# Performance work log

Hardware: AMD Instinct MI355X
Metric: run time of the kernel (lower is better)

Reference implementation:

```python
import jax, jax.numpy as jnp
import numpy as np

B, N, C = 16, 1024, 1152
H = 16
D = C // H  # 72
INNER = 4608
EPS = 1e-6


def _layernorm(x, g, b):
    mu = jnp.mean(x, axis=-1, keepdims=True)
    var = jnp.mean(jnp.square(x - mu), axis=-1, keepdims=True)
    return (x - mu) * jax.lax.rsqrt(var + EPS) * g + b


def setup_inputs() -> dict:
    key = jax.random.key(0)
    ks = jax.random.split(key, 16)
    s_c = 1.0 / np.sqrt(C)
    s_i = 1.0 / np.sqrt(INNER)
    return {
        "x": jax.random.normal(ks[0], (B, N, C), dtype=jnp.float32),
        "ln1_g": jnp.ones((C,), jnp.float32),
        "ln1_b": jnp.zeros((C,), jnp.float32),
        # weights stored (in, out) so y = x @ W + b (equiv to torch x @ W.T + b)
        "qkv_w": jax.random.normal(ks[1], (C, 3 * C), jnp.float32) * s_c,
        "qkv_b": jnp.zeros((3 * C,), jnp.float32),
        "proj_w": jax.random.normal(ks[2], (C, C), jnp.float32) * s_c,
        "proj_b": jnp.zeros((C,), jnp.float32),
        "ln2_g": jnp.ones((C,), jnp.float32),
        "ln2_b": jnp.zeros((C,), jnp.float32),
        "fc1_w": jax.random.normal(ks[3], (C, INNER), jnp.float32) * s_c,
        "fc1_b": jnp.zeros((INNER,), jnp.float32),
        "fc2_w": jax.random.normal(ks[4], (INNER, C), jnp.float32) * s_i,
        "fc2_b": jnp.zeros((C,), jnp.float32),
    }


def reference(x, ln1_g, ln1_b, qkv_w, qkv_b, proj_w, proj_b,
              ln2_g, ln2_b, fc1_w, fc1_b, fc2_w, fc2_b):
    scale = D ** -0.5
    # --- attention branch ---
    h = _layernorm(x, ln1_g, ln1_b)
    qkv = (h @ qkv_w + qkv_b).reshape(B, N, 3, H, D)
    q, k, v = jnp.moveaxis(qkv, 2, 0)            # each (B, N, H, D)
    q = q.transpose(0, 2, 1, 3)                   # (B, H, N, D)
    k = k.transpose(0, 2, 1, 3)
    v = v.transpose(0, 2, 1, 3)
    attn = jnp.einsum('bhnd,bhmd->bhnm', q, k) * scale
    attn = jax.nn.softmax(attn, axis=-1)
    out = jnp.einsum('bhnm,bhmd->bhnd', attn, v)
    out = out.transpose(0, 2, 1, 3).reshape(B, N, C)
    x = x + out @ proj_w + proj_b
    # --- MLP branch ---
    h = _layernorm(x, ln2_g, ln2_b)
    h = jax.nn.gelu(h @ fc1_w + fc1_b, approximate=False)
    x = x + h @ fc2_w + fc2_b
    return x
```

## Files before the change

### kernel.cpp

```cpp
#include <hip/hip_runtime.h>
#include <hip/hip_bf16.h>

typedef unsigned short ushort_t;
using short8 = __attribute__((ext_vector_type(8))) short;
using f32x4  = __attribute__((ext_vector_type(4))) float;

#define DEVI __device__ __forceinline__

DEVI ushort_t f2bf(float f) {
    union { float f; unsigned u; } c; c.f = f;
    unsigned u = c.u;
    return (ushort_t)((u + 0x7FFF + ((u >> 16) & 1)) >> 16);
}

DEVI f32x4 mfma16(short8 a, short8 b, f32x4 c) {
    return __builtin_amdgcn_mfma_f32_16x16x32_bf16(a, b, c, 0, 0, 0);
}

DEVI void gld16(const void* g, void* l) {
    __builtin_amdgcn_global_load_lds(
        (const __attribute__((address_space(1))) unsigned int*)g,
        (__attribute__((address_space(3))) unsigned int*)l, 16, 0, 0);
}

#define Bsz 16
#define Ntok 1024
#define Cdim 1152
#define Hn 16
#define Dh 72
#define Dp 96
#define INNER 4608
#define Mrows (Bsz * Ntok)

#define OFF_QKV_WT  ((size_t)0)
#define OFF_PROJ_WT ((size_t)7962624)
#define OFF_FC1_WT  ((size_t)10616832)
#define OFF_FC2_WT  ((size_t)21233664)
#define OFF_H       ((size_t)31850496)
#define OFF_ATT     ((size_t)69599232)
#define OFF_Q       ((size_t)107347968)
#define OFF_K       ((size_t)157679616)
#define OFF_VT      ((size_t)208011264)
#define OFF_HIDDEN  OFF_Q

__global__ __launch_bounds__(256) void transpose_cast(
    const float* __restrict__ W, ushort_t* __restrict__ Wt, int K, int N)
{
    __shared__ float t[64][65];
    const int n0 = blockIdx.x * 64;
    const int k0 = blockIdx.y * 64;
    #pragma unroll
    for (int j = 0; j < 4; ++j) {
        int idx = threadIdx.x + j * 256;
        int r = idx >> 4;
        int c4 = idx & 15;
        float4 v = *(const float4*)&W[(size_t)(k0 + r) * N + n0 + c4 * 4];
        t[r][c4 * 4 + 0] = v.x; t[r][c4 * 4 + 1] = v.y;
        t[r][c4 * 4 + 2] = v.z; t[r][c4 * 4 + 3] = v.w;
    }
    __syncthreads();
    #pragma unroll
    for (int j = 0; j < 4; ++j) {
        int idx = threadIdx.x + j * 256;
        int rn = idx >> 4;
        int c4 = idx & 15;
        ushort4 o;
        o.x = f2bf(t[c4 * 4 + 0][rn]);
        o.y = f2bf(t[c4 * 4 + 1][rn]);
        o.z = f2bf(t[c4 * 4 + 2][rn]);
        o.w = f2bf(t[c4 * 4 + 3][rn]);
        *(ushort4*)&Wt[(size_t)(n0 + rn) * K + k0 + c4 * 4] = o;
    }
}

__global__ __launch_bounds__(256) void ln_kernel(
    const float* __restrict__ x, const float* __restrict__ g,
    const float* __restrict__ b, ushort_t* __restrict__ out)
{
    const int row = blockIdx.x;
    const int tid = threadIdx.x;
    const int lane = tid & 63, wid = tid >> 6;
    const float* xr = x + (size_t)row * Cdim;

    float4 v0 = ((const float4*)xr)[tid];
    float4 v1 = {0, 0, 0, 0};
    if (tid < 32) v1 = ((const float4*)xr)[256 + tid];
    float s  = v0.x + v0.y + v0.z + v0.w + v1.x + v1.y + v1.z + v1.w;
    float s2 = v0.x*v0.x + v0.y*v0.y + v0.z*v0.z + v0.w*v0.w
             + v1.x*v1.x + v1.y*v1.y + v1.z*v1.z + v1.w*v1.w;
    #pragma unroll
    for (int off = 32; off >= 1; off >>= 1) {
        s  += __shfl_xor(s, off);
        s2 += __shfl_xor(s2, off);
    }
    __shared__ float red[8];
    if (lane == 0) { red[wid] = s; red[4 + wid] = s2; }
    __syncthreads();
    s  = red[0] + red[1] + red[2] + red[3];
    s2 = red[4] + red[5] + red[6] + red[7];
    const float mu = s * (1.0f / Cdim);
    const float var = s2 * (1.0f / Cdim) - mu * mu;
    const float rs = rsqrtf(var + 1e-6f);

    ushort_t* orow = out + (size_t)row * Cdim;
    {
        float4 g4 = ((const float4*)g)[tid];
        float4 b4 = ((const float4*)b)[tid];
        ushort4 o;
        o.x = f2bf((v0.x - mu) * rs * g4.x + b4.x);
        o.y = f2bf((v0.y - mu) * rs * g4.y + b4.y);
        o.z = f2bf((v0.z - mu) * rs * g4.z + b4.z);
        o.w = f2bf((v0.w - mu) * rs * g4.w + b4.w);
        ((ushort4*)orow)[tid] = o;
    }
    if (tid < 32) {
        float4 g4 = ((const float4*)g)[256 + tid];
        float4 b4 = ((const float4*)b)[256 + tid];
        ushort4 o;
        o.x = f2bf((v1.x - mu) * rs * g4.x + b4.x);
        o.y = f2bf((v1.y - mu) * rs * g4.y + b4.y);
        o.z = f2bf((v1.z - mu) * rs * g4.z + b4.z);
        o.w = f2bf((v1.w - mu) * rs * g4.w + b4.w);
        ((ushort4*)orow)[256 + tid] = o;
    }
}

enum { EPI_QKV = 0, EPI_PROJ = 1, EPI_FC1 = 2, EPI_FC2 = 3 };

template<int EPI, int N, int K>
__global__ __launch_bounds__(256) void gemm_bt(
    const ushort_t* __restrict__ A, const ushort_t* __restrict__ Bt,
    const float* __restrict__ bias, const float* __restrict__ resid,
    float* __restrict__ outf, ushort_t* __restrict__ outb,
    ushort_t* __restrict__ outq, ushort_t* __restrict__ outk, ushort_t* __restrict__ outv)
{
    __shared__ ushort_t As[128 * 32];
    __shared__ ushort_t Bs[128 * 32];
    const int tid = threadIdx.x;
    const int lane = tid & 63, wid = tid >> 6;
    const int m0 = blockIdx.y * 128;
    const int n0 = blockIdx.x * 128;
    const int fr = lane & 15, fq = lane >> 4;

    f32x4 acc[4][4] = {};

    const int srow = lane >> 2;
    const int scol = (lane & 3) * 8;
    const ushort_t* Ag = A + (size_t)m0 * K;
    const ushort_t* Bg = Bt + (size_t)n0 * K;

    for (int kk = 0; kk < K; kk += 32) {
        #pragma unroll
        for (int j = 0; j < 2; ++j) {
            const int crow = wid * 32 + j * 16;
            gld16(Ag + (size_t)(crow + srow) * K + kk + scol, &As[crow * 32]);
            gld16(Bg + (size_t)(crow + srow) * K + kk + scol, &Bs[crow * 32]);
        }
        __syncthreads();
        short8 af[4], bfr[4];
        #pragma unroll
        for (int mi = 0; mi < 4; ++mi)
            af[mi] = *(const short8*)&As[((wid >> 1) * 64 + mi * 16 + fr) * 32 + fq * 8];
        #pragma unroll
        for (int ni = 0; ni < 4; ++ni)
            bfr[ni] = *(const short8*)&Bs[((wid & 1) * 64 + ni * 16 + fr) * 32 + fq * 8];
        #pragma unroll
        for (int mi = 0; mi < 4; ++mi)
            #pragma unroll
            for (int ni = 0; ni < 4; ++ni)
                acc[mi][ni] = mfma16(af[mi], bfr[ni], acc[mi][ni]);
        __syncthreads();
    }

    #pragma unroll
    for (int mi = 0; mi < 4; ++mi) {
        #pragma unroll
        for (int ni = 0; ni < 4; ++ni) {
            const int col = n0 + (wid & 1) * 64 + ni * 16 + fr;
            const int rbase = m0 + (wid >> 1) * 64 + mi * 16 + fq * 4;
            #pragma unroll
            for (int i = 0; i < 4; ++i) {
                const int r = rbase + i;
                float v = acc[mi][ni][i];
                if (EPI == EPI_QKV) {
                    v += bias[col];
                    const int which = col / Cdim;
                    const int rc = col % Cdim;
                    const int h = rc / Dh, d = rc % Dh;
                    const int b = r >> 10, n = r & 1023;
                    const size_t head = (size_t)(b * Hn + h);
                    if (which == 0)      outq[(head * Ntok + n) * Dp + d] = f2bf(v);
                    else if (which == 1) outk[(head * Ntok + n) * Dp + d] = f2bf(v);
                    else                 outv[(head * Dp + d) * Ntok + n] = f2bf(v);
                } else if (EPI == EPI_PROJ) {
                    v += bias[col] + resid[(size_t)r * N + col];
                    outf[(size_t)r * N + col] = v;
                } else if (EPI == EPI_FC1) {
                    v += bias[col];
                    v = 0.5f * v * (1.0f + erff(v * 0.70710678118f));
                    outb[(size_t)r * N + col] = f2bf(v);
                } else {
                    v += bias[col] + outf[(size_t)r * N + col];
                    outf[(size_t)r * N + col] = v;
                }
            }
        }
    }
}

__global__ __launch_bounds__(256) void attn_kernel(
    const ushort_t* __restrict__ q, const ushort_t* __restrict__ k,
    const ushort_t* __restrict__ vt, ushort_t* __restrict__ out)
{
    const int tid = threadIdx.x;
    const int lane = tid & 63, wid = tid >> 6;
    const int bh = blockIdx.y;
    const int qbase = blockIdx.x * 128 + wid * 32;
    const int fr = lane & 15, fq = lane >> 4;
    const ushort_t* qh = q  + (size_t)bh * Ntok * Dp;
    const ushort_t* kh = k  + (size_t)bh * Ntok * Dp;
    const ushort_t* vh = vt + (size_t)bh * Dp * Ntok;

    short8 aq[2][3];
    #pragma unroll
    for (int t = 0; t < 2; ++t)
        #pragma unroll
        for (int ks = 0; ks < 3; ++ks)
            aq[t][ks] = *(const short8*)&qh[(size_t)(qbase + t * 16 + fr) * Dp + ks * 32 + fq * 8];

    f32x4 o[2][5] = {};
    float mrun[2][4], lsum[2][4];
    #pragma unroll
    for (int t = 0; t < 2; ++t)
        #pragma unroll
        for (int i = 0; i < 4; ++i) { mrun[t][i] = -1e30f; lsum[t][i] = 0.0f; }

    __shared__ ushort_t plds[4][2][16][32];
    const float scale = 0.117851130f;

    for (int kv = 0; kv < Ntok; kv += 32) {
        short8 kb0[3], kb1[3], bv[5];
        #pragma unroll
        for (int ks = 0; ks < 3; ++ks) {
            kb0[ks] = *(const short8*)&kh[(size_t)(kv + fr) * Dp + ks * 32 + fq * 8];
            kb1[ks] = *(const short8*)&kh[(size_t)(kv + 16 + fr) * Dp + ks * 32 + fq * 8];
        }
        #pragma unroll
        for (int dt = 0; dt < 5; ++dt)
            bv[dt] = *(const short8*)&vh[(size_t)(dt * 16 + fr) * Ntok + kv + fq * 8];

        f32x4 s[2][2] = {};
        __builtin_amdgcn_s_setprio(1);
        #pragma unroll
        for (int ks = 0; ks < 3; ++ks)
            #pragma unroll
            for (int t = 0; t < 2; ++t) {
                s[t][0] = mfma16(aq[t][ks], kb0[ks], s[t][0]);
                s[t][1] = mfma16(aq[t][ks], kb1[ks], s[t][1]);
            }
        __builtin_amdgcn_s_setprio(0);

        #pragma unroll
        for (int t = 0; t < 2; ++t) {
            float a0[4], a1[4];
            float lmax = -1e30f;
            #pragma unroll
            for (int i = 0; i < 4; ++i) {
                a0[i] = s[t][0][i] * scale;
                a1[i] = s[t][1][i] * scale;
                lmax = fmaxf(lmax, fmaxf(a0[i], a1[i]));
            }
            const float mmin = fminf(fminf(mrun[t][0], mrun[t][1]),
                                     fminf(mrun[t][2], mrun[t][3]));
            if (!__all(lmax <= mmin + 8.0f)) {
                #pragma unroll
                for (int i = 0; i < 4; ++i) {
                    float mx = fmaxf(a0[i], a1[i]);
                    mx = fmaxf(mx, __shfl_xor(mx, 1));
                    mx = fmaxf(mx, __shfl_xor(mx, 2));
                    mx = fmaxf(mx, __shfl_xor(mx, 4));
                    mx = fmaxf(mx, __shfl_xor(mx, 8));
                    const float mnew = fmaxf(mrun[t][i], mx);
                    const float f = __expf(mrun[t][i] - mnew);
                    mrun[t][i] = mnew;
                    lsum[t][i] *= f;
                    #pragma unroll
                    for (int dt = 0; dt < 5; ++dt) o[t][dt][i] *= f;
                }
            }
            #pragma unroll
            for (int i = 0; i < 4; ++i) {
                float p0 = __expf(a0[i] - mrun[t][i]);
                float p1 = __expf(a1[i] - mrun[t][i]);
                lsum[t][i] += p0 + p1;
                plds[wid][t][fq * 4 + i][fr]      = f2bf(p0);
                plds[wid][t][fq * 4 + i][16 + fr] = f2bf(p1);
            }
        }
        short8 pa[2];
        #pragma unroll
        for (int t = 0; t < 2; ++t)
            pa[t] = *(const short8*)&plds[wid][t][fr][fq * 8];
        __builtin_amdgcn_s_setprio(1);
        #pragma unroll
        for (int dt = 0; dt < 5; ++dt)
            #pragma unroll
            for (int t = 0; t < 2; ++t)
                o[t][dt] = mfma16(pa[t], bv[dt], o[t][dt]);
        __builtin_amdgcn_s_setprio(0);
    }

    const int b = bh >> 4, h = bh & 15;
    #pragma unroll
    for (int t = 0; t < 2; ++t) {
        float inv[4];
        #pragma unroll
        for (int i = 0; i < 4; ++i) {
            float s = lsum[t][i];
            s += __shfl_xor(s, 1);
            s += __shfl_xor(s, 2);
            s += __shfl_xor(s, 4);
            s += __shfl_xor(s, 8);
            inv[i] = 1.0f / s;
        }
        #pragma unroll
        for (int dt = 0; dt < 5; ++dt) {
            const int d = dt * 16 + fr;
            if (d < Dh) {
                #pragma unroll
                for (int i = 0; i < 4; ++i) {
                    const size_t idx = ((size_t)(b * Ntok) + qbase + t * 16 + fq * 4 + i) * Cdim + h * Dh + d;
                    out[idx] = f2bf(o[t][dt][i] * inv[i]);
                }
            }
        }
    }
}

extern "C" void kernel_launch(void* const* d_in, const int* in_sizes, int n_in,
                              void* d_out, int out_size, void* d_ws, size_t ws_size,
                              hipStream_t stream) {
    const float* x      = (const float*)d_in[0];
    const float* ln1_g  = (const float*)d_in[1];
    const float* ln1_b  = (const float*)d_in[2];
    const float* qkv_w  = (const float*)d_in[3];
    const float* qkv_b  = (const float*)d_in[4];
    const float* proj_w = (const float*)d_in[5];
    const float* proj_b = (const float*)d_in[6];
    const float* ln2_g  = (const float*)d_in[7];
    const float* ln2_b  = (const float*)d_in[8];
    const float* fc1_w  = (const float*)d_in[9];
    const float* fc1_b  = (const float*)d_in[10];
    const float* fc2_w  = (const float*)d_in[11];
    const float* fc2_b  = (const float*)d_in[12];

    char* ws = (char*)d_ws;
    ushort_t* qkv_wT  = (ushort_t*)(ws + OFF_QKV_WT);
    ushort_t* proj_wT = (ushort_t*)(ws + OFF_PROJ_WT);
    ushort_t* fc1_wT  = (ushort_t*)(ws + OFF_FC1_WT);
    ushort_t* fc2_wT  = (ushort_t*)(ws + OFF_FC2_WT);
    ushort_t* hbuf    = (ushort_t*)(ws + OFF_H);
    ushort_t* attnout = (ushort_t*)(ws + OFF_ATT);
    ushort_t* qb      = (ushort_t*)(ws + OFF_Q);
    ushort_t* kb      = (ushort_t*)(ws + OFF_K);
    ushort_t* vtb     = (ushort_t*)(ws + OFF_VT);
    ushort_t* hidden  = (ushort_t*)(ws + OFF_HIDDEN);
    float* out = (float*)d_out;

    hipMemsetAsync(ws + OFF_Q, 0, (size_t)3 * 50331648, stream);

    transpose_cast<<<dim3(3 * Cdim / 64, Cdim / 64), 256, 0, stream>>>(qkv_w, qkv_wT, Cdim, 3 * Cdim);
    transpose_cast<<<dim3(Cdim / 64, Cdim / 64), 256, 0, stream>>>(proj_w, proj_wT, Cdim, Cdim);
    transpose_cast<<<dim3(INNER / 64, Cdim / 64), 256, 0, stream>>>(fc1_w, fc1_wT, Cdim, INNER);
    transpose_cast<<<dim3(Cdim / 64, INNER / 64), 256, 0, stream>>>(fc2_w, fc2_wT, INNER, Cdim);

    ln_kernel<<<Mrows, 256, 0, stream>>>(x, ln1_g, ln1_b, hbuf);

    gemm_bt<EPI_QKV, 3 * Cdim, Cdim><<<dim3(27, 128), 256, 0, stream>>>(
        hbuf, qkv_wT, qkv_b, nullptr, nullptr, nullptr, qb, kb, vtb);

    attn_kernel<<<dim3(Ntok / 128, Bsz * Hn), 256, 0, stream>>>(qb, kb, vtb, attnout);

    gemm_bt<EPI_PROJ, Cdim, Cdim><<<dim3(9, 128), 256, 0, stream>>>(
        attnout, proj_wT, proj_b, x, out, nullptr, nullptr, nullptr, nullptr);

    ln_kernel<<<Mrows, 256, 0, stream>>>(out, ln2_g, ln2_b, hbuf);

    gemm_bt<EPI_FC1, INNER, Cdim><<<dim3(36, 128), 256, 0, stream>>>(
        hbuf, fc1_wT, fc1_b, nullptr, nullptr, hidden, nullptr, nullptr, nullptr);

    gemm_bt<EPI_FC2, Cdim, INNER><<<dim3(9, 128), 256, 0, stream>>>(
        hidden, fc2_wT, fc2_b, nullptr, out, nullptr, nullptr, nullptr, nullptr);
}
```

Baseline: 1.233 ms.

## Rework GEMM to 256x128x64 tiles with triple-buffered async LDS pipeline and swizzle

The bf16 GEMM kernel now uses 512-thread blocks with 256x128 output tiles and a K-step of 64. Global-to-LDS loads are triple-buffered so the loads for tile t+2 are in flight while tile t is computed, using explicit vmcnt waits. The LDS layout is XOR-swizzled to avoid bank conflicts, and MFMA issue runs at raised priority. The aim is to hide memory latency and cut barrier overhead and LDS traffic per FLOP, at the cost of 144KB of LDS per block, which limits occupancy, and more intricate synchronization.

```diff
diff --git a/kernel.cpp b/kernel.cpp
--- a/kernel.cpp
+++ b/kernel.cpp
@@ -127,57 +127,113 @@
 
 enum { EPI_QKV = 0, EPI_PROJ = 1, EPI_FC1 = 2, EPI_FC2 = 3 };
 
+#define TBM 256
+#define TBN 128
+#define TBK 64
+#define BUFB 49152
+
 template<int EPI, int N, int K>
-__global__ __launch_bounds__(256) void gemm_bt(
+__global__ __launch_bounds__(512, 2) void gemm_bt(
     const ushort_t* __restrict__ A, const ushort_t* __restrict__ Bt,
     const float* __restrict__ bias, const float* __restrict__ resid,
     float* __restrict__ outf, ushort_t* __restrict__ outb,
     ushort_t* __restrict__ outq, ushort_t* __restrict__ outk, ushort_t* __restrict__ outv)
 {
-    __shared__ ushort_t As[128 * 32];
-    __shared__ ushort_t Bs[128 * 32];
+    __shared__ ushort_t smem[3 * BUFB / 2];
     const int tid = threadIdx.x;
     const int lane = tid & 63, wid = tid >> 6;
-    const int m0 = blockIdx.y * 128;
-    const int n0 = blockIdx.x * 128;
+    const int wr = wid >> 1, wc = wid & 1;
     const int fr = lane & 15, fq = lane >> 4;
-
-    f32x4 acc[4][4] = {};
-
-    const int srow = lane >> 2;
-    const int scol = (lane & 3) * 8;
+    const int m0 = blockIdx.y * TBM;
+    const int n0 = blockIdx.x * TBN;
+
     const ushort_t* Ag = A + (size_t)m0 * K;
     const ushort_t* Bg = Bt + (size_t)n0 * K;
 
-    for (int kk = 0; kk < K; kk += 32) {
-        #pragma unroll
-        for (int j = 0; j < 2; ++j) {
-            const int crow = wid * 32 + j * 16;
-            gld16(Ag + (size_t)(crow + srow) * K + kk + scol, &As[crow * 32]);
-            gld16(Bg + (size_t)(crow + srow) * K + kk + scol, &Bs[crow * 32]);
-        }
-        __syncthreads();
-        short8 af[4], bfr[4];
-        #pragma unroll
-        for (int mi = 0; mi < 4; ++mi)
-            af[mi] = *(const short8*)&As[((wid >> 1) * 64 + mi * 16 + fr) * 32 + fq * 8];
-        #pragma unroll
-        for (int ni = 0; ni < 4; ++ni)
-            bfr[ni] = *(const short8*)&Bs[((wid & 1) * 64 + ni * 16 + fr) * 32 + fq * 8];
-        #pragma unroll
-        for (int mi = 0; mi < 4; ++mi)
-            #pragma unroll
-            for (int ni = 0; ni < 4; ++ni)
-                acc[mi][ni] = mfma16(af[mi], bfr[ni], acc[mi][ni]);
-        __syncthreads();
-    }
+    size_t srcA[4]; int dstA[4];
+    #pragma unroll
+    for (int r = 0; r < 4; ++r) {
+        const int chunk = r * 512 + tid;
+        const int row = chunk >> 3;
+        const int slot = chunk & 7;
+        srcA[r] = (size_t)row * K + (slot ^ (row & 7)) * 8;
+        dstA[r] = (r * 512 + wid * 64) * 16;
+    }
+    size_t srcB[2]; int dstB[2];
+    #pragma unroll
+    for (int r = 0; r < 2; ++r) {
+        const int chunk = r * 512 + tid;
+        const int row = chunk >> 3;
+        const int slot = chunk & 7;
+        srcB[r] = (size_t)row * K + (slot ^ (row & 7)) * 8;
+        dstB[r] = 32768 + (r * 512 + wid * 64) * 16;
+    }
+
+    auto STAGE = [&](int buf, int kk) {
+        char* lb = (char*)smem + (size_t)buf * BUFB;
+        #pragma unroll
+        for (int r = 0; r < 4; ++r) gld16(Ag + srcA[r] + kk, lb + dstA[r]);
+        #pragma unroll
+        for (int r = 0; r < 2; ++r) gld16(Bg + srcB[r] + kk, lb + dstB[r]);
+    };
+
+    const int swz = (fr & 7) << 4;
+    int aoff[4][2], boff[4][2];
+    #pragma unroll
+    for (int i = 0; i < 4; ++i)
+        #pragma unroll
+        for (int kh = 0; kh < 2; ++kh) {
+            const int rowA = wr * 64 + i * 16 + fr;
+            aoff[i][kh] = rowA * 128 + ((kh * 64 + fq * 16) ^ swz);
+            const int rowB = wc * 64 + i * 16 + fr;
+            boff[i][kh] = 32768 + rowB * 128 + ((kh * 64 + fq * 16) ^ swz);
+        }
+
+    f32x4 acc[4][4] = {};
+    const int NT = K / TBK;
+
+    STAGE(0, 0);
+    STAGE(1, TBK);
+
+    auto COMPUTE = [&](int t) {
+        const char* lb = (const char*)smem + (size_t)(t % 3) * BUFB;
+        #pragma unroll
+        for (int kh = 0; kh < 2; ++kh) {
+            short8 a[4], b[4];
+            #pragma unroll
+            for (int i = 0; i < 4; ++i) {
+                a[i] = *(const short8*)(lb + aoff[i][kh]);
+                b[i] = *(const short8*)(lb + boff[i][kh]);
+            }
+            __builtin_amdgcn_s_setprio(1);
+            #pragma unroll
+            for (int mi = 0; mi < 4; ++mi)
+                #pragma unroll
+                for (int ni = 0; ni < 4; ++ni)
+                    acc[mi][ni] = mfma16(a[mi], b[ni], acc[mi][ni]);
+            __builtin_amdgcn_s_setprio(0);
+        }
+    };
+
+    for (int t = 0; t < NT - 1; ++t) {
+        asm volatile("s_waitcnt vmcnt(6)" ::: "memory");
+        __builtin_amdgcn_s_barrier();
+        __builtin_amdgcn_sched_barrier(0);
+        if (t + 2 < NT) STAGE((t + 2) % 3, (t + 2) * TBK);
+        __builtin_amdgcn_sched_barrier(0);
+        COMPUTE(t);
+    }
+    asm volatile("s_waitcnt vmcnt(0)" ::: "memory");
+    __builtin_amdgcn_s_barrier();
+    __builtin_amdgcn_sched_barrier(0);
+    COMPUTE(NT - 1);
 
     #pragma unroll
     for (int mi = 0; mi < 4; ++mi) {
         #pragma unroll
         for (int ni = 0; ni < 4; ++ni) {
-            const int col = n0 + (wid & 1) * 64 + ni * 16 + fr;
-            const int rbase = m0 + (wid >> 1) * 64 + mi * 16 + fq * 4;
+            const int col = n0 + wc * 64 + ni * 16 + fr;
+            const int rbase = m0 + wr * 64 + mi * 16 + fq * 4;
             #pragma unroll
             for (int i = 0; i < 4; ++i) {
                 const int r = rbase + i;
@@ -376,19 +432,19 @@
 
     ln_kernel<<<Mrows, 256, 0, stream>>>(x, ln1_g, ln1_b, hbuf);
 
-    gemm_bt<EPI_QKV, 3 * Cdim, Cdim><<<dim3(27, 128), 256, 0, stream>>>(
+    gemm_bt<EPI_QKV, 3 * Cdim, Cdim><<<dim3(27, Mrows / TBM), 512, 0, stream>>>(
         hbuf, qkv_wT, qkv_b, nullptr, nullptr, nullptr, qb, kb, vtb);
 
     attn_kernel<<<dim3(Ntok / 128, Bsz * Hn), 256, 0, stream>>>(qb, kb, vtb, attnout);
 
-    gemm_bt<EPI_PROJ, Cdim, Cdim><<<dim3(9, 128), 256, 0, stream>>>(
+    gemm_bt<EPI_PROJ, Cdim, Cdim><<<dim3(9, Mrows / TBM), 512, 0, stream>>>(
         attnout, proj_wT, proj_b, x, out, nullptr, nullptr, nullptr, nullptr);
 
     ln_kernel<<<Mrows, 256, 0, stream>>>(out, ln2_g, ln2_b, hbuf);
 
-    gemm_bt<EPI_FC1, INNER, Cdim><<<dim3(36, 128), 256, 0, stream>>>(
+    gemm_bt<EPI_FC1, INNER, Cdim><<<dim3(36, Mrows / TBM), 512, 0, stream>>>(
         hbuf, fc1_wT, fc1_b, nullptr, nullptr, hidden, nullptr, nullptr, nullptr);
 
-    gemm_bt<EPI_FC2, Cdim, INNER><<<dim3(9, 128), 256, 0, stream>>>(
+    gemm_bt<EPI_FC2, Cdim, INNER><<<dim3(9, Mrows / TBM), 512, 0, stream>>>(
         hidden, fc2_wT, fc2_b, nullptr, out, nullptr, nullptr, nullptr, nullptr);
 }
```

After: 1.133 ms. 8.1% less time.
